# Optimization experiments

Hardware: AMD Instinct MI355X
Metric: run time of the kernel (lower is better)

Reference implementation:

```python
import jax, jax.numpy as jnp
import numpy as np

ALPHA = 1.5
A = 0.5
BANDWIDTH = 1.0
SPHERE_RADIUS = 1.0
HIDDEN = 1024
HEAD = 64
EPS_ACOS = 1e-07
EPS_NORM = 1e-12  # torch F.normalize clamp_min eps


def _l2norm(v):
    # F.normalize(v, p=2, dim=-1)
    n = jnp.sqrt(jnp.sum(v * v, axis=-1, keepdims=True))
    return v / jnp.maximum(n, EPS_NORM)


def setup_inputs() -> dict:
    key = jax.random.key(0)
    ks = jax.random.split(key, 7)
    B, S = 8, 2048
    s = 1.0 / np.sqrt(HIDDEN)
    return {
        "x": jax.random.normal(ks[0], (B, S, HIDDEN), dtype=jnp.float32),
        "Wq": jax.random.uniform(ks[1], (HIDDEN, HEAD), jnp.float32, -s, s),
        "bq": jax.random.uniform(ks[2], (HEAD,), jnp.float32, -s, s),
        "Wk": jax.random.uniform(ks[3], (HIDDEN, HEAD), jnp.float32, -s, s),
        "bk": jax.random.uniform(ks[4], (HEAD,), jnp.float32, -s, s),
        "Wv": jax.random.uniform(ks[5], (HIDDEN, HEAD), jnp.float32, -s, s),
        "bv": jax.random.uniform(ks[6], (HEAD,), jnp.float32, -s, s),
    }


def reference(x, Wq, bq, Wk, bk, Wv, bv):
    # q,k,v: [B,S,HEAD], L2-normalized along feature axis
    q = _l2norm(jnp.einsum("bsh,hd->bsd", x, Wq) + bq)
    k = _l2norm(jnp.einsum("bsh,hd->bsd", x, Wk) + bk)
    v = _l2norm(jnp.einsum("bsh,hd->bsd", x, Wv) + bv)

    # geodesic distance on sphere: [B,S,S]
    cos = jnp.einsum("bqd,bkd->bqk", q, k)
    g_dist = jnp.arccos(jnp.clip(cos, -1.0 + EPS_ACOS, 1.0 - EPS_ACOS)) * SPHERE_RADIUS

    # alpha < 2 -> power-law score
    score = (1.0 + g_dist / jnp.sqrt(BANDWIDTH)) ** (-HEAD - ALPHA)

    # dual degree normalization (a != 0): diag(row^-a) @ S @ diag(col^-a),
    # expressed as broadcast row/col scaling (same math, no diag_embed matmuls)
    r = jnp.sum(score, axis=-1) ** (-A)  # [B,Sq]
    c = jnp.sum(score, axis=-2) ** (-A)  # [B,Sk]
    k_tilde = r[..., :, None] * score * c[..., None, :]

    # L1 normalize over key axis (F.normalize p=1): entries are positive
    denom = jnp.maximum(jnp.sum(jnp.abs(k_tilde), axis=-1, keepdims=True), EPS_NORM)
    probs = k_tilde / denom

    out = jnp.einsum("bqk,bkd->bqd", probs, v)
    return (out, probs)
```

## Files before the change

### kernel.cpp

```cpp
#include <hip/hip_runtime.h>
#include <math.h>

#define BB 8
#define SS 2048
#define HH 1024
#define DD 64
#define NCV 65

typedef __attribute__((ext_vector_type(8))) short bf16x8;
typedef __attribute__((ext_vector_type(4))) float f32x4;

#define MFMA16(a, b, c) __builtin_amdgcn_mfma_f32_16x16x32_bf16(a, b, c, 0, 0, 0)

__device__ __forceinline__ ushort bf16rne(float f) {
    uint u = __float_as_uint(f);
    uint r = (u + 0x7FFFu + ((u >> 16) & 1u)) >> 16;
    return (ushort)r;
}
__device__ __forceinline__ float bf2f(ushort h) {
    return __uint_as_float(((uint)h) << 16);
}

__device__ __forceinline__ float score_fn(float cosv) {
    float ax = fminf(fabsf(cosv), 1.0f - 1e-7f);
    float p = fmaf(ax, -0.0012624911f, 0.0066700901f);
    p = fmaf(ax, p, -0.0170881256f);
    p = fmaf(ax, p, 0.0308918810f);
    p = fmaf(ax, p, -0.0501743046f);
    p = fmaf(ax, p, 0.0889789874f);
    p = fmaf(ax, p, -0.2145988016f);
    p = fmaf(ax, p, 1.5707963050f);
    float r = sqrtf(1.0f - ax) * p;
    float g = (cosv >= 0.0f) ? r : (3.14159265358979f - r);
    return exp2f(-65.5f * log2f(1.0f + g));
}

__global__ __launch_bounds__(256) void k_prep(
    const float* __restrict__ Wq, const float* __restrict__ Wk, const float* __restrict__ Wv,
    const float* __restrict__ bq, const float* __restrict__ bk, const float* __restrict__ bv,
    ushort* __restrict__ Whi, ushort* __restrict__ Wlo, float* __restrict__ bcat)
{
    const int n = blockIdx.x;
    const int m = n >> 6, d = n & 63;
    const float* W = (m == 0) ? Wq : (m == 1 ? Wk : Wv);
    #pragma unroll
    for (int i = 0; i < 4; ++i) {
        int j = i * 256 + threadIdx.x;
        float f = W[(size_t)j * DD + d];
        ushort h = bf16rne(f);
        Whi[(size_t)n * HH + j] = h;
        Wlo[(size_t)n * HH + j] = bf16rne(f - bf2f(h));
    }
    if (n == 0 && threadIdx.x < 192) {
        int t = threadIdx.x, mm = t >> 6, dd = t & 63;
        const float* b = (mm == 0) ? bq : (mm == 1 ? bk : bv);
        bcat[t] = b[dd];
    }
}

__global__ __launch_bounds__(256) void k_projmm(
    const float* __restrict__ x, const ushort* __restrict__ Whi,
    const ushort* __restrict__ Wlo, const float* __restrict__ bcat,
    ushort* __restrict__ qh, ushort* __restrict__ ql,
    ushort* __restrict__ kh, ushort* __restrict__ kl,
    float* __restrict__ vw)
{
    __shared__ __align__(16) char smem[32 * 193 * 4];
    __shared__ float rns[96];
    __shared__ float bsh[192];
    ushort* xhi = (ushort*)smem;
    ushort* xlo = xhi + 32 * 128;
    float* ctile = (float*)smem;

    const int t = threadIdx.x;
    const int lane = t & 63;
    const int wid = t >> 6;
    const int row0 = blockIdx.x * 32;
    if (t < 192) bsh[t] = bcat[t];

    f32x4 acc[2][3];
    #pragma unroll
    for (int ar = 0; ar < 2; ++ar)
        #pragma unroll
        for (int bc = 0; bc < 3; ++bc)
            acc[ar][bc] = (f32x4){0.f, 0.f, 0.f, 0.f};

    for (int ch = 0; ch < 8; ++ch) {
        const int j0 = ch * 128;
        __syncthreads();
        #pragma unroll
        for (int i = 0; i < 2; ++i) {
            int u = i * 256 + t;
            int row = u >> 4, uc = u & 15;
            const float* xp = &x[(size_t)(row0 + row) * HH + j0 + uc * 8];
            float4 a = *(const float4*)xp;
            float4 b = *(const float4*)(xp + 4);
            float fs[8] = {a.x, a.y, a.z, a.w, b.x, b.y, b.z, b.w};
            bf16x8 hv, lv;
            #pragma unroll
            for (int e = 0; e < 8; ++e) {
                ushort h = bf16rne(fs[e]);
                hv[e] = (short)h;
                lv[e] = (short)bf16rne(fs[e] - bf2f(h));
            }
            int su = uc ^ (row & 7);
            *(bf16x8*)(xhi + row * 128 + su * 8) = hv;
            *(bf16x8*)(xlo + row * 128 + su * 8) = lv;
        }
        __syncthreads();
        #pragma unroll
        for (int ks = 0; ks < 4; ++ks) {
            bf16x8 ah[2], al[2], bh[3], bl[3];
            #pragma unroll
            for (int ar = 0; ar < 2; ++ar) {
                int row = ar * 16 + (lane & 15);
                int su = (ks * 4 + (lane >> 4)) ^ (row & 7);
                ah[ar] = *(const bf16x8*)(xhi + row * 128 + su * 8);
                al[ar] = *(const bf16x8*)(xlo + row * 128 + su * 8);
            }
            const int koff = j0 + ks * 32 + (lane >> 4) * 8;
            #pragma unroll
            for (int bc = 0; bc < 3; ++bc) {
                int n = wid * 48 + bc * 16 + (lane & 15);
                bh[bc] = *(const bf16x8*)(Whi + (size_t)n * HH + koff);
                bl[bc] = *(const bf16x8*)(Wlo + (size_t)n * HH + koff);
            }
            #pragma unroll
            for (int ar = 0; ar < 2; ++ar)
                #pragma unroll
                for (int bc = 0; bc < 3; ++bc) {
                    acc[ar][bc] = MFMA16(ah[ar], bh[bc], acc[ar][bc]);
                    acc[ar][bc] = MFMA16(ah[ar], bl[bc], acc[ar][bc]);
                    acc[ar][bc] = MFMA16(al[ar], bh[bc], acc[ar][bc]);
                }
        }
    }
    __syncthreads();
    #pragma unroll
    for (int ar = 0; ar < 2; ++ar)
        #pragma unroll
        for (int bc = 0; bc < 3; ++bc) {
            int n = wid * 48 + bc * 16 + (lane & 15);
            #pragma unroll
            for (int r = 0; r < 4; ++r) {
                int row = ar * 16 + (lane >> 4) * 4 + r;
                ctile[row * 193 + n] = acc[ar][bc][r];
            }
        }
    __syncthreads();
    if (t < 96) {
        int mat = t >> 5, row = t & 31;
        float ss = 0.f;
        #pragma unroll 8
        for (int d = 0; d < 64; ++d) {
            float v = ctile[row * 193 + mat * 64 + d] + bsh[mat * 64 + d];
            ss = fmaf(v, v, ss);
        }
        rns[t] = 1.0f / fmaxf(sqrtf(ss), 1e-12f);
    }
    __syncthreads();
    #pragma unroll
    for (int i = 0; i < 24; ++i) {
        int idx = i * 256 + t;
        int row = idx / 192;
        int n = idx - row * 192;
        float v = (ctile[row * 193 + n] + bsh[n]) * rns[(n >> 6) * 32 + row];
        size_t off = (size_t)(row0 + row) * DD + (n & 63);
        if (n < 64) {
            ushort h = bf16rne(v);
            qh[off] = h; ql[off] = bf16rne(v - bf2f(h));
        } else if (n < 128) {
            ushort h = bf16rne(v);
            kh[off] = h; kl[off] = bf16rne(v - bf2f(h));
        } else {
            vw[off] = v;
        }
    }
}

__global__ __launch_bounds__(256, 4) void k_score(
    const ushort* __restrict__ qh, const ushort* __restrict__ ql,
    const ushort* __restrict__ kh, const ushort* __restrict__ kl,
    ushort* __restrict__ scrS)
{
    const int t = threadIdx.x;
    const int lane = t & 63;
    const int w = t >> 6;
    const int bid = blockIdx.x;
    const int b  = bid >> 8;
    const int q0 = ((bid >> 1) & 127) * 16;
    const int kbase = (bid & 1) * 1024 + w * 256;
    const int qn = lane & 15;
    const int g = lane >> 4;

    bf16x8 qbh[2], qbl[2];
    #pragma unroll
    for (int ks = 0; ks < 2; ++ks) {
        size_t off = (size_t)(b * SS + q0 + qn) * DD + ks * 32 + g * 8;
        qbh[ks] = *(const bf16x8*)(qh + off);
        qbl[ks] = *(const bf16x8*)(ql + off);
    }
    ushort* srow = scrS + (size_t)(b * SS + q0 + qn) * 4096 + 2048;

    #pragma unroll 2
    for (int kt = 0; kt < 8; ++kt) {
        const int ks0 = kbase + kt * 32;
        size_t roffA = (size_t)(b * SS + ks0 + qn) * DD + g * 8;
        size_t roffB = roffA + (size_t)16 * DD;
        bf16x8 kah0 = *(const bf16x8*)(kh + roffA);
        bf16x8 kal0 = *(const bf16x8*)(kl + roffA);
        bf16x8 kah1 = *(const bf16x8*)(kh + roffA + 32);
        bf16x8 kal1 = *(const bf16x8*)(kl + roffA + 32);
        bf16x8 kbh0 = *(const bf16x8*)(kh + roffB);
        bf16x8 kbl0 = *(const bf16x8*)(kl + roffB);
        bf16x8 kbh1 = *(const bf16x8*)(kh + roffB + 32);
        bf16x8 kbl1 = *(const bf16x8*)(kl + roffB + 32);
        f32x4 aT0 = (f32x4){0.f, 0.f, 0.f, 0.f}, aT1 = aT0;
        aT0 = MFMA16(kah0, qbh[0], aT0);  aT1 = MFMA16(kbh0, qbh[0], aT1);
        aT0 = MFMA16(kah1, qbh[1], aT0);  aT1 = MFMA16(kbh1, qbh[1], aT1);
        aT0 = MFMA16(kah0, qbl[0], aT0);  aT1 = MFMA16(kbh0, qbl[0], aT1);
        aT0 = MFMA16(kah1, qbl[1], aT0);  aT1 = MFMA16(kbh1, qbl[1], aT1);
        aT0 = MFMA16(kal0, qbh[0], aT0);  aT1 = MFMA16(kbl0, qbh[0], aT1);
        aT0 = MFMA16(kal1, qbh[1], aT0);  aT1 = MFMA16(kbl1, qbh[1], aT1);

        const int kc0 = ks0 + g * 4;
        uint2 wv0, wv1;
        wv0.x = (uint)bf16rne(score_fn(aT0[0])) | ((uint)bf16rne(score_fn(aT0[1])) << 16);
        wv0.y = (uint)bf16rne(score_fn(aT0[2])) | ((uint)bf16rne(score_fn(aT0[3])) << 16);
        wv1.x = (uint)bf16rne(score_fn(aT1[0])) | ((uint)bf16rne(score_fn(aT1[1])) << 16);
        wv1.y = (uint)bf16rne(score_fn(aT1[2])) | ((uint)bf16rne(score_fn(aT1[3])) << 16);
        *(uint2*)(srow + kc0) = wv0;
        *(uint2*)(srow + kc0 + 16) = wv1;
    }
}

__global__ __launch_bounds__(256) void k_csum_cvc(
    const ushort* __restrict__ scrS, const float* __restrict__ vw,
    ushort* __restrict__ cvT)
{
    __shared__ float cls[32][64];
    __shared__ float csh[64];
    __shared__ float vsT[64][65];
    const int t = threadIdx.x;
    const int b = blockIdx.x >> 5;
    const int k0 = (blockIdx.x & 31) * 64;

    {
        const int tq = t >> 3, tk = t & 7;
        float colacc[8];
        #pragma unroll
        for (int e = 0; e < 8; ++e) colacc[e] = 0.f;
        #pragma unroll 4
        for (int it = 0; it < 64; ++it) {
            int q = it * 32 + tq;
            bf16x8 s8 = *(const bf16x8*)(scrS + (size_t)(b * SS + q) * 4096 + 2048 + k0 + tk * 8);
            #pragma unroll
            for (int e = 0; e < 8; ++e) colacc[e] += bf2f((ushort)s8[e]);
        }
        #pragma unroll
        for (int e = 0; e < 8; ++e) cls[tq][tk * 8 + e] = colacc[e];
    }
    __syncthreads();
    if (t < 64) {
        float s = 0.f;
        #pragma unroll
        for (int tq = 0; tq < 32; ++tq) s += cls[tq][t];
        csh[t] = 1.0f / sqrtf(s);
    }
    {
        const int j = t & 63, rr = t >> 6;
        #pragma unroll
        for (int it = 0; it < 16; ++it) {
            int kk = it * 4 + rr;
            vsT[j][kk] = vw[(size_t)(b * SS + k0 + kk) * DD + j];
        }
    }
    __syncthreads();
    {
        const int kk4 = (t & 15) * 4;
        #pragma unroll
        for (int jt = 0; jt < 4; ++jt) {
            int j = jt * 16 + (t >> 4);
            uint2 wv;
            wv.x = (uint)bf16rne(csh[kk4 + 0] * vsT[j][kk4 + 0])
                 | ((uint)bf16rne(csh[kk4 + 1] * vsT[j][kk4 + 1]) << 16);
            wv.y = (uint)bf16rne(csh[kk4 + 2] * vsT[j][kk4 + 2])
                 | ((uint)bf16rne(csh[kk4 + 3] * vsT[j][kk4 + 3]) << 16);
            *(uint2*)(cvT + ((size_t)b * NCV + j) * SS + k0 + kk4) = wv;
        }
        if (t < 16) {
            uint2 wv;
            wv.x = (uint)bf16rne(csh[t * 4 + 0]) | ((uint)bf16rne(csh[t * 4 + 1]) << 16);
            wv.y = (uint)bf16rne(csh[t * 4 + 2]) | ((uint)bf16rne(csh[t * 4 + 3]) << 16);
            *(uint2*)(cvT + ((size_t)b * NCV + 64) * SS + k0 + t * 4);
            *(uint2*)(cvT + ((size_t)b * NCV + 64) * SS + k0 + t * 4) = wv;
        }
    }
}

__global__ __launch_bounds__(256, 4) void k_final(
    const ushort* __restrict__ scrS, const ushort* __restrict__ cvT,
    float* __restrict__ probs, float* __restrict__ out)
{
    __shared__ float nred[16][64];
    __shared__ float dPart[4][16];
    __shared__ float dInv[16];
    const int t = threadIdx.x;
    const int lane = t & 63;
    const int w = t >> 6;
    const int b = blockIdx.x >> 7;
    const int q0 = (blockIdx.x & 127) * 16;
    const int kbase = w * 512;
    const int qn = lane & 15;
    const int g = lane >> 4;

    ((float*)nred)[t] = 0.f; ((float*)nred)[t + 256] = 0.f;
    ((float*)nred)[t + 512] = 0.f; ((float*)nred)[t + 768] = 0.f;

    const ushort* cslice = cvT + (size_t)b * NCV * SS;
    const ushort* cbrow = cslice + (size_t)64 * SS;
    const ushort* srow = scrS + (size_t)(b * SS + q0 + qn) * 4096 + 2048;

    float dacc = 0.f;
    f32x4 nacc[4];
    #pragma unroll
    for (int ct = 0; ct < 4; ++ct) nacc[ct] = (f32x4){0.f, 0.f, 0.f, 0.f};

    #pragma unroll 2
    for (int ch = 0; ch < 16; ++ch) {
        const int ks0 = kbase + ch * 32;
        bf16x8 s8 = *(const bf16x8*)(srow + ks0 + g * 8);
        bf16x8 c8 = *(const bf16x8*)(cbrow + ks0 + g * 8);
        #pragma unroll
        for (int e = 0; e < 8; ++e)
            dacc = fmaf(bf2f((ushort)s8[e]), bf2f((ushort)c8[e]), dacc);
        #pragma unroll
        for (int ct = 0; ct < 4; ++ct) {
            bf16x8 bfv = *(const bf16x8*)(cslice + (size_t)(ct * 16 + qn) * SS + ks0 + g * 8);
            nacc[ct] = MFMA16(s8, bfv, nacc[ct]);
        }
    }
    {
        float d = dacc;
        d += __shfl_xor(d, 16, 64);
        d += __shfl_xor(d, 32, 64);
        if (lane < 16) dPart[w][lane] = d;
    }
    __syncthreads();
    if (t < 16) dInv[t] = 1.0f / (dPart[0][t] + dPart[1][t] + dPart[2][t] + dPart[3][t]);
    #pragma unroll
    for (int ct = 0; ct < 4; ++ct)
        #pragma unroll
        for (int r = 0; r < 4; ++r)
            atomicAdd(&nred[g * 4 + r][ct * 16 + qn], nacc[ct][r]);
    __syncthreads();
    {
        int q = t >> 4, c4 = (t & 15) * 4;
        float di = dInv[q];
        float4 o;
        o.x = nred[q][c4] * di;     o.y = nred[q][c4 + 1] * di;
        o.z = nred[q][c4 + 2] * di; o.w = nred[q][c4 + 3] * di;
        *(float4*)&out[(size_t)(b * SS + q0 + q) * DD + c4] = o;
    }
    float cf[8];
    {
        bf16x8 c8 = *(const bf16x8*)(cbrow + t * 8);
        #pragma unroll
        for (int e = 0; e < 8; ++e) cf[e] = bf2f((ushort)c8[e]);
    }
    for (int r = 0; r < 16; ++r) {
        bf16x8 s8 = *(const bf16x8*)(scrS + (size_t)(b * SS + q0 + r) * 4096 + 2048 + t * 8);
        float di = dInv[r];
        __syncthreads();
        float4 o0, o1;
        o0.x = bf2f((ushort)s8[0]) * cf[0] * di;
        o0.y = bf2f((ushort)s8[1]) * cf[1] * di;
        o0.z = bf2f((ushort)s8[2]) * cf[2] * di;
        o0.w = bf2f((ushort)s8[3]) * cf[3] * di;
        o1.x = bf2f((ushort)s8[4]) * cf[4] * di;
        o1.y = bf2f((ushort)s8[5]) * cf[5] * di;
        o1.z = bf2f((ushort)s8[6]) * cf[6] * di;
        o1.w = bf2f((ushort)s8[7]) * cf[7] * di;
        float* prow = probs + (size_t)(b * SS + q0 + r) * SS + t * 8;
        *(float4*)prow = o0;
        *(float4*)(prow + 4) = o1;
    }
}

extern "C" void kernel_launch(void* const* d_in, const int* in_sizes, int n_in,
                              void* d_out, int out_size, void* d_ws, size_t ws_size,
                              hipStream_t stream)
{
    const float* x  = (const float*)d_in[0];
    const float* Wq = (const float*)d_in[1];
    const float* bq = (const float*)d_in[2];
    const float* Wk = (const float*)d_in[3];
    const float* bk = (const float*)d_in[4];
    const float* Wv = (const float*)d_in[5];
    const float* bv = (const float*)d_in[6];

    float* out   = (float*)d_out;
    float* probs = out + (size_t)BB * SS * DD;
    ushort* scrS = (ushort*)probs;

    const size_t NQ = (size_t)BB * SS * DD;
    ushort* qh    = (ushort*)d_ws;
    ushort* ql    = qh + NQ;
    ushort* kh    = ql + NQ;
    ushort* kl    = kh + NQ;
    float*  vw    = (float*)(kl + NQ);
    ushort* cvT   = (ushort*)(vw + NQ);
    ushort* Whi   = cvT + (size_t)BB * NCV * SS;
    ushort* Wlo   = Whi + (size_t)192 * HH;
    float*  bcat  = (float*)(Wlo + (size_t)192 * HH);

    k_prep    <<<192, 256, 0, stream>>>(Wq, Wk, Wv, bq, bk, bv, Whi, Wlo, bcat);
    k_projmm  <<<512, 256, 0, stream>>>(x, Whi, Wlo, bcat, qh, ql, kh, kl, vw);
    k_score   <<<2048, 256, 0, stream>>>(qh, ql, kh, kl, scrS);
    k_csum_cvc<<<256, 256, 0, stream>>>(scrS, vw, cvT);
    k_final   <<<1024, 256, 0, stream>>>(scrS, cvT, probs, out);
}
```

Baseline: 223.2 us.

## Switch score and final kernels to 32x32 MFMA tiles with software-pipelined K loads

Measured after the change: 221.6 us. No clear change (-0.7%).

```diff
diff --git a/kernel.cpp b/kernel.cpp
--- a/kernel.cpp
+++ b/kernel.cpp
@@ -9,8 +9,10 @@
 
 typedef __attribute__((ext_vector_type(8))) short bf16x8;
 typedef __attribute__((ext_vector_type(4))) float f32x4;
+typedef __attribute__((ext_vector_type(16))) float f32x16;
 
 #define MFMA16(a, b, c) __builtin_amdgcn_mfma_f32_16x16x32_bf16(a, b, c, 0, 0, 0)
+#define MFMA32(a, b, c) __builtin_amdgcn_mfma_f32_32x32x16_bf16(a, b, c, 0, 0, 0)
 
 __device__ __forceinline__ ushort bf16rne(float f) {
     uint u = __float_as_uint(f);
@@ -178,6 +180,35 @@
     }
 }
 
+#define K_LOAD(H0,H1,H2,H3,L0,L1,L2,L3, KT) { \
+    const ushort* kp = kh + (size_t)(b * SS + kbase + (KT) * 32 + qrow) * DD + kg; \
+    const ushort* lp = kl + (size_t)(b * SS + kbase + (KT) * 32 + qrow) * DD + kg; \
+    H0 = *(const bf16x8*)(kp);      L0 = *(const bf16x8*)(lp); \
+    H1 = *(const bf16x8*)(kp + 16); L1 = *(const bf16x8*)(lp + 16); \
+    H2 = *(const bf16x8*)(kp + 32); L2 = *(const bf16x8*)(lp + 32); \
+    H3 = *(const bf16x8*)(kp + 48); L3 = *(const bf16x8*)(lp + 48); }
+
+#define K_COMPUTE(H0,H1,H2,H3,L0,L1,L2,L3, KT) { \
+    f32x16 acc = Z16; \
+    acc = MFMA32(H0, qbh0, acc); acc = MFMA32(H0, qbl0, acc); acc = MFMA32(L0, qbh0, acc); \
+    acc = MFMA32(H1, qbh1, acc); acc = MFMA32(H1, qbl1, acc); acc = MFMA32(L1, qbh1, acc); \
+    acc = MFMA32(H2, qbh2, acc); acc = MFMA32(H2, qbl2, acc); acc = MFMA32(L2, qbh2, acc); \
+    acc = MFMA32(H3, qbh3, acc); acc = MFMA32(H3, qbl3, acc); acc = MFMA32(L3, qbh3, acc); \
+    const int kloc = kbase + (KT) * 32 + hi4; \
+    uint2 wv; \
+    wv.x = (uint)bf16rne(score_fn(acc[0]))  | ((uint)bf16rne(score_fn(acc[1]))  << 16); \
+    wv.y = (uint)bf16rne(score_fn(acc[2]))  | ((uint)bf16rne(score_fn(acc[3]))  << 16); \
+    *(uint2*)(srow + kloc) = wv; \
+    wv.x = (uint)bf16rne(score_fn(acc[4]))  | ((uint)bf16rne(score_fn(acc[5]))  << 16); \
+    wv.y = (uint)bf16rne(score_fn(acc[6]))  | ((uint)bf16rne(score_fn(acc[7]))  << 16); \
+    *(uint2*)(srow + kloc + 8) = wv; \
+    wv.x = (uint)bf16rne(score_fn(acc[8]))  | ((uint)bf16rne(score_fn(acc[9]))  << 16); \
+    wv.y = (uint)bf16rne(score_fn(acc[10])) | ((uint)bf16rne(score_fn(acc[11])) << 16); \
+    *(uint2*)(srow + kloc + 16) = wv; \
+    wv.x = (uint)bf16rne(score_fn(acc[12])) | ((uint)bf16rne(score_fn(acc[13])) << 16); \
+    wv.y = (uint)bf16rne(score_fn(acc[14])) | ((uint)bf16rne(score_fn(acc[15])) << 16); \
+    *(uint2*)(srow + kloc + 24) = wv; }
+
 __global__ __launch_bounds__(256, 4) void k_score(
     const ushort* __restrict__ qh, const ushort* __restrict__ ql,
     const ushort* __restrict__ kh, const ushort* __restrict__ kl,
@@ -188,50 +219,34 @@
     const int w = t >> 6;
     const int bid = blockIdx.x;
     const int b  = bid >> 8;
-    const int q0 = ((bid >> 1) & 127) * 16;
-    const int kbase = (bid & 1) * 1024 + w * 256;
-    const int qn = lane & 15;
-    const int g = lane >> 4;
-
-    bf16x8 qbh[2], qbl[2];
-    #pragma unroll
-    for (int ks = 0; ks < 2; ++ks) {
-        size_t off = (size_t)(b * SS + q0 + qn) * DD + ks * 32 + g * 8;
-        qbh[ks] = *(const bf16x8*)(qh + off);
-        qbl[ks] = *(const bf16x8*)(ql + off);
-    }
-    ushort* srow = scrS + (size_t)(b * SS + q0 + qn) * 4096 + 2048;
-
-    #pragma unroll 2
-    for (int kt = 0; kt < 8; ++kt) {
-        const int ks0 = kbase + kt * 32;
-        size_t roffA = (size_t)(b * SS + ks0 + qn) * DD + g * 8;
-        size_t roffB = roffA + (size_t)16 * DD;
-        bf16x8 kah0 = *(const bf16x8*)(kh + roffA);
-        bf16x8 kal0 = *(const bf16x8*)(kl + roffA);
-        bf16x8 kah1 = *(const bf16x8*)(kh + roffA + 32);
-        bf16x8 kal1 = *(const bf16x8*)(kl + roffA + 32);
-        bf16x8 kbh0 = *(const bf16x8*)(kh + roffB);
-        bf16x8 kbl0 = *(const bf16x8*)(kl + roffB);
-        bf16x8 kbh1 = *(const bf16x8*)(kh + roffB + 32);
-        bf16x8 kbl1 = *(const bf16x8*)(kl + roffB + 32);
-        f32x4 aT0 = (f32x4){0.f, 0.f, 0.f, 0.f}, aT1 = aT0;
-        aT0 = MFMA16(kah0, qbh[0], aT0);  aT1 = MFMA16(kbh0, qbh[0], aT1);
-        aT0 = MFMA16(kah1, qbh[1], aT0);  aT1 = MFMA16(kbh1, qbh[1], aT1);
-        aT0 = MFMA16(kah0, qbl[0], aT0);  aT1 = MFMA16(kbh0, qbl[0], aT1);
-        aT0 = MFMA16(kah1, qbl[1], aT0);  aT1 = MFMA16(kbh1, qbl[1], aT1);
-        aT0 = MFMA16(kal0, qbh[0], aT0);  aT1 = MFMA16(kbl0, qbh[0], aT1);
-        aT0 = MFMA16(kal1, qbh[1], aT0);  aT1 = MFMA16(kbl1, qbh[1], aT1);
-
-        const int kc0 = ks0 + g * 4;
-        uint2 wv0, wv1;
-        wv0.x = (uint)bf16rne(score_fn(aT0[0])) | ((uint)bf16rne(score_fn(aT0[1])) << 16);
-        wv0.y = (uint)bf16rne(score_fn(aT0[2])) | ((uint)bf16rne(score_fn(aT0[3])) << 16);
-        wv1.x = (uint)bf16rne(score_fn(aT1[0])) | ((uint)bf16rne(score_fn(aT1[1])) << 16);
-        wv1.y = (uint)bf16rne(score_fn(aT1[2])) | ((uint)bf16rne(score_fn(aT1[3])) << 16);
-        *(uint2*)(srow + kc0) = wv0;
-        *(uint2*)(srow + kc0 + 16) = wv1;
-    }
+    const int q0 = ((bid >> 2) & 63) * 32;
+    const int kbase = (bid & 3) * 512 + w * 128;
+    const int qrow = lane & 31;
+    const int kg = (lane >> 5) * 8;
+    const int hi4 = (lane >> 5) * 4;
+    const f32x16 Z16 = {0.f,0.f,0.f,0.f,0.f,0.f,0.f,0.f,0.f,0.f,0.f,0.f,0.f,0.f,0.f,0.f};
+
+    const size_t qoff = (size_t)(b * SS + q0 + qrow) * DD + kg;
+    bf16x8 qbh0 = *(const bf16x8*)(qh + qoff);
+    bf16x8 qbh1 = *(const bf16x8*)(qh + qoff + 16);
+    bf16x8 qbh2 = *(const bf16x8*)(qh + qoff + 32);
+    bf16x8 qbh3 = *(const bf16x8*)(qh + qoff + 48);
+    bf16x8 qbl0 = *(const bf16x8*)(ql + qoff);
+    bf16x8 qbl1 = *(const bf16x8*)(ql + qoff + 16);
+    bf16x8 qbl2 = *(const bf16x8*)(ql + qoff + 32);
+    bf16x8 qbl3 = *(const bf16x8*)(ql + qoff + 48);
+    ushort* srow = scrS + (size_t)(b * SS + q0 + qrow) * 4096 + 2048;
+
+    bf16x8 xh0, xh1, xh2, xh3, xl0, xl1, xl2, xl3;
+    bf16x8 yh0, yh1, yh2, yh3, yl0, yl1, yl2, yl3;
+    K_LOAD(xh0,xh1,xh2,xh3,xl0,xl1,xl2,xl3, 0)
+    K_LOAD(yh0,yh1,yh2,yh3,yl0,yl1,yl2,yl3, 1)
+    K_COMPUTE(xh0,xh1,xh2,xh3,xl0,xl1,xl2,xl3, 0)
+    K_LOAD(xh0,xh1,xh2,xh3,xl0,xl1,xl2,xl3, 2)
+    K_COMPUTE(yh0,yh1,yh2,yh3,yl0,yl1,yl2,yl3, 1)
+    K_LOAD(yh0,yh1,yh2,yh3,yl0,yl1,yl2,yl3, 3)
+    K_COMPUTE(xh0,xh1,xh2,xh3,xl0,xl1,xl2,xl3, 2)
+    K_COMPUTE(yh0,yh1,yh2,yh3,yl0,yl1,yl2,yl3, 3)
 }
 
 __global__ __launch_bounds__(256) void k_csum_cvc(
@@ -292,7 +307,6 @@
             uint2 wv;
             wv.x = (uint)bf16rne(csh[t * 4 + 0]) | ((uint)bf16rne(csh[t * 4 + 1]) << 16);
             wv.y = (uint)bf16rne(csh[t * 4 + 2]) | ((uint)bf16rne(csh[t * 4 + 3]) << 16);
-            *(uint2*)(cvT + ((size_t)b * NCV + 64) * SS + k0 + t * 4);
             *(uint2*)(cvT + ((size_t)b * NCV + 64) * SS + k0 + t * 4) = wv;
         }
     }
@@ -302,65 +316,68 @@
     const ushort* __restrict__ scrS, const ushort* __restrict__ cvT,
     float* __restrict__ probs, float* __restrict__ out)
 {
-    __shared__ float nred[16][64];
-    __shared__ float dPart[4][16];
-    __shared__ float dInv[16];
+    __shared__ float nred[32][64];
+    __shared__ float dPart[4][32];
+    __shared__ float dInv[32];
     const int t = threadIdx.x;
     const int lane = t & 63;
     const int w = t >> 6;
-    const int b = blockIdx.x >> 7;
-    const int q0 = (blockIdx.x & 127) * 16;
+    const int b = blockIdx.x >> 6;
+    const int q0 = (blockIdx.x & 63) * 32;
     const int kbase = w * 512;
-    const int qn = lane & 15;
-    const int g = lane >> 4;
-
-    ((float*)nred)[t] = 0.f; ((float*)nred)[t + 256] = 0.f;
-    ((float*)nred)[t + 512] = 0.f; ((float*)nred)[t + 768] = 0.f;
+    const int qrow = lane & 31;
+    const int kg = (lane >> 5) * 8;
+    const f32x16 Z16 = {0.f,0.f,0.f,0.f,0.f,0.f,0.f,0.f,0.f,0.f,0.f,0.f,0.f,0.f,0.f,0.f};
+
+    #pragma unroll
+    for (int i = 0; i < 8; ++i) ((float*)nred)[t + i * 256] = 0.f;
+    __syncthreads();
 
     const ushort* cslice = cvT + (size_t)b * NCV * SS;
     const ushort* cbrow = cslice + (size_t)64 * SS;
-    const ushort* srow = scrS + (size_t)(b * SS + q0 + qn) * 4096 + 2048;
+    const ushort* srow = scrS + (size_t)(b * SS + q0 + qrow) * 4096 + 2048;
 
     float dacc = 0.f;
-    f32x4 nacc[4];
-    #pragma unroll
-    for (int ct = 0; ct < 4; ++ct) nacc[ct] = (f32x4){0.f, 0.f, 0.f, 0.f};
-
-    #pragma unroll 2
-    for (int ch = 0; ch < 16; ++ch) {
-        const int ks0 = kbase + ch * 32;
-        bf16x8 s8 = *(const bf16x8*)(srow + ks0 + g * 8);
-        bf16x8 c8 = *(const bf16x8*)(cbrow + ks0 + g * 8);
+    f32x16 n0 = Z16, n1 = Z16;
+
+    #pragma unroll 4
+    for (int ch = 0; ch < 32; ++ch) {
+        const int kc = kbase + ch * 16 + kg;
+        bf16x8 s8 = *(const bf16x8*)(srow + kc);
+        bf16x8 c8 = *(const bf16x8*)(cbrow + kc);
+        bf16x8 b0 = *(const bf16x8*)(cslice + (size_t)qrow * SS + kc);
+        bf16x8 b1 = *(const bf16x8*)(cslice + (size_t)(32 + qrow) * SS + kc);
         #pragma unroll
         for (int e = 0; e < 8; ++e)
             dacc = fmaf(bf2f((ushort)s8[e]), bf2f((ushort)c8[e]), dacc);
-        #pragma unroll
-        for (int ct = 0; ct < 4; ++ct) {
-            bf16x8 bfv = *(const bf16x8*)(cslice + (size_t)(ct * 16 + qn) * SS + ks0 + g * 8);
-            nacc[ct] = MFMA16(s8, bfv, nacc[ct]);
-        }
+        n0 = MFMA32(s8, b0, n0);
+        n1 = MFMA32(s8, b1, n1);
     }
     {
         float d = dacc;
-        d += __shfl_xor(d, 16, 64);
         d += __shfl_xor(d, 32, 64);
-        if (lane < 16) dPart[w][lane] = d;
-    }
-    __syncthreads();
-    if (t < 16) dInv[t] = 1.0f / (dPart[0][t] + dPart[1][t] + dPart[2][t] + dPart[3][t]);
-    #pragma unroll
-    for (int ct = 0; ct < 4; ++ct)
-        #pragma unroll
-        for (int r = 0; r < 4; ++r)
-            atomicAdd(&nred[g * 4 + r][ct * 16 + qn], nacc[ct][r]);
-    __syncthreads();
-    {
-        int q = t >> 4, c4 = (t & 15) * 4;
+        if (lane < 32) dPart[w][lane] = d;
+    }
+    __syncthreads();
+    if (t < 32) dInv[t] = 1.0f / (dPart[0][t] + dPart[1][t] + dPart[2][t] + dPart[3][t]);
+    #pragma unroll
+    for (int r = 0; r < 16; ++r) {
+        int q = (r & 3) + 8 * (r >> 2) + 4 * (lane >> 5);
+        atomicAdd(&nred[q][qrow], n0[r]);
+        atomicAdd(&nred[q][32 + qrow], n1[r]);
+    }
+    __syncthreads();
+    {
+        int q = t >> 3, d0 = (t & 7) * 8;
         float di = dInv[q];
-        float4 o;
-        o.x = nred[q][c4] * di;     o.y = nred[q][c4 + 1] * di;
-        o.z = nred[q][c4 + 2] * di; o.w = nred[q][c4 + 3] * di;
-        *(float4*)&out[(size_t)(b * SS + q0 + q) * DD + c4] = o;
+        float4 o0, o1;
+        o0.x = nred[q][d0 + 0] * di; o0.y = nred[q][d0 + 1] * di;
+        o0.z = nred[q][d0 + 2] * di; o0.w = nred[q][d0 + 3] * di;
+        o1.x = nred[q][d0 + 4] * di; o1.y = nred[q][d0 + 5] * di;
+        o1.z = nred[q][d0 + 6] * di; o1.w = nred[q][d0 + 7] * di;
+        float* op = &out[(size_t)(b * SS + q0 + q) * DD + d0];
+        *(float4*)op = o0;
+        *(float4*)(op + 4) = o1;
     }
     float cf[8];
     {
@@ -368,22 +385,32 @@
         #pragma unroll
         for (int e = 0; e < 8; ++e) cf[e] = bf2f((ushort)c8[e]);
     }
-    for (int r = 0; r < 16; ++r) {
-        bf16x8 s8 = *(const bf16x8*)(scrS + (size_t)(b * SS + q0 + r) * 4096 + 2048 + t * 8);
-        float di = dInv[r];
+#define P_STORE(S8, DI, RR) { \
+    float4 o0, o1; \
+    o0.x = bf2f((ushort)S8[0]) * cf[0] * DI; \
+    o0.y = bf2f((ushort)S8[1]) * cf[1] * DI; \
+    o0.z = bf2f((ushort)S8[2]) * cf[2] * DI; \
+    o0.w = bf2f((ushort)S8[3]) * cf[3] * DI; \
+    o1.x = bf2f((ushort)S8[4]) * cf[4] * DI; \
+    o1.y = bf2f((ushort)S8[5]) * cf[5] * DI; \
+    o1.z = bf2f((ushort)S8[6]) * cf[6] * DI; \
+    o1.w = bf2f((ushort)S8[7]) * cf[7] * DI; \
+    float* prow = probs + (size_t)(b * SS + q0 + (RR)) * SS + t * 8; \
+    *(float4*)prow = o0; \
+    *(float4*)(prow + 4) = o1; }
+
+    #pragma unroll
+    for (int r0 = 0; r0 < 32; r0 += 4) {
+        bf16x8 sA = *(const bf16x8*)(scrS + (size_t)(b * SS + q0 + r0 + 0) * 4096 + 2048 + t * 8);
+        bf16x8 sB = *(const bf16x8*)(scrS + (size_t)(b * SS + q0 + r0 + 1) * 4096 + 2048 + t * 8);
+        bf16x8 sC = *(const bf16x8*)(scrS + (size_t)(b * SS + q0 + r0 + 2) * 4096 + 2048 + t * 8);
+        bf16x8 sD = *(const bf16x8*)(scrS + (size_t)(b * SS + q0 + r0 + 3) * 4096 + 2048 + t * 8);
+        float dA = dInv[r0 + 0], dB = dInv[r0 + 1], dC = dInv[r0 + 2], dD = dInv[r0 + 3];
         __syncthreads();
-        float4 o0, o1;
-        o0.x = bf2f((ushort)s8[0]) * cf[0] * di;
-        o0.y = bf2f((ushort)s8[1]) * cf[1] * di;
-        o0.z = bf2f((ushort)s8[2]) * cf[2] * di;
-        o0.w = bf2f((ushort)s8[3]) * cf[3] * di;
-        o1.x = bf2f((ushort)s8[4]) * cf[4] * di;
-        o1.y = bf2f((ushort)s8[5]) * cf[5] * di;
-        o1.z = bf2f((ushort)s8[6]) * cf[6] * di;
-        o1.w = bf2f((ushort)s8[7]) * cf[7] * di;
-        float* prow = probs + (size_t)(b * SS + q0 + r) * SS + t * 8;
-        *(float4*)prow = o0;
-        *(float4*)(prow + 4) = o1;
+        P_STORE(sA, dA, r0 + 0)
+        P_STORE(sB, dB, r0 + 1)
+        P_STORE(sC, dC, r0 + 2)
+        P_STORE(sD, dD, r0 + 3)
     }
 }
 
@@ -418,5 +445,5 @@
     k_projmm  <<<512, 256, 0, stream>>>(x, Whi, Wlo, bcat, qh, ql, kh, kl, vw);
     k_score   <<<2048, 256, 0, stream>>>(qh, ql, kh, kl, scrS);
     k_csum_cvc<<<256, 256, 0, stream>>>(scrS, vw, cvT);
-    k_final   <<<1024, 256, 0, stream>>>(scrS, cvT, probs, out);
-}
+    k_final   <<<512, 256, 0, stream>>>(scrS, cvT, probs, out);
+}
```
